# Kernel optimization log

Hardware: AMD Instinct MI355X
Metric: run time of the kernel (lower is better)

## Reference

```python
import jax, jax.numpy as jnp
import numpy as np

B, K, C, G = 8192, 4096, 4096, 32
EPS = 1e-5


def setup_inputs() -> dict:
    key = jax.random.key(0)
    ks = jax.random.split(key, 4)
    x = jax.random.normal(ks[0], (B, K), dtype=jnp.float32)
    weight = jax.random.normal(ks[1], (C, K), dtype=jnp.float32) * (1.0 / np.sqrt(K))
    bias = jax.random.normal(ks[2], (C,), dtype=jnp.float32) * 0.02
    gn_weight = jnp.ones((C,), dtype=jnp.float32)
    gn_bias = jnp.zeros((C,), dtype=jnp.float32)
    multiply_weight = jax.random.normal(ks[3], (C,), dtype=jnp.float32)
    return {"x": x, "weight": weight, "bias": bias, "gn_weight": gn_weight,
            "gn_bias": gn_bias, "multiply_weight": multiply_weight}


def reference(x, weight, bias, gn_weight, gn_bias, multiply_weight):
    # Linear: y = x @ W^T + b   -> [B, C]
    h = jnp.einsum('bk,ck->bc', x, weight) + bias
    # GroupNorm over each group of C//G channels, per sample
    hg = h.reshape(B, G, C // G)
    mean = jnp.mean(hg, axis=-1, keepdims=True)
    var = jnp.mean(jnp.square(hg), axis=-1, keepdims=True) - jnp.square(mean)
    hn = ((hg - mean) * jax.lax.rsqrt(var + EPS)).reshape(B, C)
    hn = hn * gn_weight + gn_bias
    # Swish -> * multiply_weight -> Swish
    x1 = hn * jax.nn.sigmoid(hn)
    x2 = x1 * multiply_weight
    return x2 * jax.nn.sigmoid(x2)
```

## Files before the change

kernel.cpp:

```cpp
#include <hip/hip_runtime.h>


typedef short bf16x8 __attribute__((ext_vector_type(8)));
typedef unsigned short u16x8 __attribute__((ext_vector_type(8)));
typedef unsigned short u16x4 __attribute__((ext_vector_type(4)));
typedef float fx4 __attribute__((ext_vector_type(4)));

__device__ __forceinline__ unsigned short f2bf(float f) {
    union { float f; unsigned u; } v; v.f = f;
    unsigned r = v.u + 0x7FFFu + ((v.u >> 16) & 1u);
    return (unsigned short)(r >> 16);
}

__device__ __forceinline__ void load_lds16(const void* g, void* l) {
    __builtin_amdgcn_global_load_lds(
        (const __attribute__((address_space(1))) void*)g,
        (__attribute__((address_space(3))) void*)l, 16, 0, 0);
}

__global__ void __launch_bounds__(256)
cvt_f32_bf16(const float* __restrict__ src, unsigned short* __restrict__ dst, long long n) {
    long long i = ((long long)blockIdx.x * 256 + threadIdx.x) * 8;
    if (i >= n) return;
    float4 a = *(const float4*)(src + i);
    float4 b = *(const float4*)(src + i + 4);
    u16x8 o;
    o[0] = f2bf(a.x); o[1] = f2bf(a.y); o[2] = f2bf(a.z); o[3] = f2bf(a.w);
    o[4] = f2bf(b.x); o[5] = f2bf(b.y); o[6] = f2bf(b.z); o[7] = f2bf(b.w);
    *(u16x8*)(dst + i) = o;
}

__device__ __forceinline__ void
epilogue(fx4 (&acc)[4][4],
         const float* __restrict__ bias, const float* __restrict__ gnw,
         const float* __restrict__ gnb,  const float* __restrict__ mw,
         float* __restrict__ out, int m0, int n0,
         int wm, int wn, int lrow, int q,
         float (*redS)[128], float (*redQ)[128]) {
    constexpr int C = 4096;
    float bia[4], gw[4], gb[4], mwv[4];
    int cidx[4];
    #pragma unroll
    for (int nt = 0; nt < 4; nt++) {
        int c = n0 + wn * 64 + nt * 16 + lrow;
        cidx[nt] = c;
        bia[nt] = bias[c]; gw[nt] = gnw[c]; gb[nt] = gnb[c]; mwv[nt] = mw[c];
    }
    #pragma unroll
    for (int mt = 0; mt < 4; mt++)
        #pragma unroll
        for (int nt = 0; nt < 4; nt++)
            #pragma unroll
            for (int r = 0; r < 4; r++)
                acc[mt][nt][r] += bia[nt];

    float s[4][4], ss[4][4];
    #pragma unroll
    for (int mt = 0; mt < 4; mt++)
        #pragma unroll
        for (int r = 0; r < 4; r++) {
            float a = 0.f, b = 0.f;
            #pragma unroll
            for (int nt = 0; nt < 4; nt++) {
                float v = acc[mt][nt][r];
                a += v; b += v * v;
            }
            s[mt][r] = a; ss[mt][r] = b;
        }
    #pragma unroll
    for (int off = 1; off < 16; off <<= 1)
        #pragma unroll
        for (int mt = 0; mt < 4; mt++)
            #pragma unroll
            for (int r = 0; r < 4; r++) {
                s[mt][r]  += __shfl_xor(s[mt][r],  off, 64);
                ss[mt][r] += __shfl_xor(ss[mt][r], off, 64);
            }
    if (lrow == 0) {
        #pragma unroll
        for (int mt = 0; mt < 4; mt++)
            #pragma unroll
            for (int r = 0; r < 4; r++) {
                int row = wm * 64 + mt * 16 + q * 4 + r;
                redS[wn][row] = s[mt][r];
                redQ[wn][row] = ss[mt][r];
            }
    }
    __syncthreads();

    #pragma unroll
    for (int mt = 0; mt < 4; mt++)
        #pragma unroll
        for (int r = 0; r < 4; r++) {
            int row = wm * 64 + mt * 16 + q * 4 + r;
            float tot  = redS[0][row] + redS[1][row];
            float tq   = redQ[0][row] + redQ[1][row];
            float mean = tot * (1.0f / 128.0f);
            float var  = tq * (1.0f / 128.0f) - mean * mean;
            s[mt][r]  = mean;
            ss[mt][r] = rsqrtf(var + 1e-5f);
        }

    #pragma unroll
    for (int mt = 0; mt < 4; mt++)
        #pragma unroll
        for (int r = 0; r < 4; r++) {
            size_t row = (size_t)(m0 + wm * 64 + mt * 16 + q * 4 + r);
            #pragma unroll
            for (int nt = 0; nt < 4; nt++) {
                float h  = acc[mt][nt][r];
                float hn = (h - s[mt][r]) * ss[mt][r];
                hn = hn * gw[nt] + gb[nt];
                float x1 = hn / (1.0f + __expf(-hn));
                float x2 = x1 * mwv[nt];
                float y  = x2 / (1.0f + __expf(-x2));
                out[row * (size_t)C + cidx[nt]] = y;
            }
        }
}

__global__ void __launch_bounds__(256)
gemm_bf16(const unsigned short* __restrict__ X,
          const unsigned short* __restrict__ Wt,
          const float* __restrict__ bias, const float* __restrict__ gnw,
          const float* __restrict__ gnb,  const float* __restrict__ mw,
          float* __restrict__ out)
{
    constexpr int K = 4096;
    __shared__ __align__(16) unsigned short As[128 * 32];
    __shared__ __align__(16) unsigned short Bs[128 * 32];
    __shared__ float redS[2][128];
    __shared__ float redQ[2][128];

    const int tid  = threadIdx.x;
    const int wave = tid >> 6;
    const int lane = tid & 63;
    const int wm = wave >> 1, wn = wave & 1;
    const int lrow = lane & 15;
    const int q    = lane >> 4;

    const int m0 = blockIdx.y * 128;
    const int n0 = blockIdx.x * 128;

    const int r0 = tid >> 2;
    const int kk = (tid & 3) * 8;
    const unsigned short* pA0 = X  + (size_t)(m0 + r0) * K + kk;
    const unsigned short* pA1 = X  + (size_t)(m0 + 64 + r0) * K + kk;
    const unsigned short* pB0 = Wt + (size_t)(n0 + r0) * K + kk;
    const unsigned short* pB1 = Wt + (size_t)(n0 + 64 + r0) * K + kk;
    unsigned short* ldsA0 = &As[wave * 512];
    unsigned short* ldsA1 = &As[2048 + wave * 512];
    unsigned short* ldsB0 = &Bs[wave * 512];
    unsigned short* ldsB1 = &Bs[2048 + wave * 512];

    fx4 acc[4][4];
    const fx4 zero = {0.f, 0.f, 0.f, 0.f};
    #pragma unroll
    for (int i = 0; i < 4; i++)
        #pragma unroll
        for (int j = 0; j < 4; j++) acc[i][j] = zero;

    for (int k0 = 0; k0 < K; k0 += 32) {
        load_lds16(pA0 + k0, ldsA0);
        load_lds16(pA1 + k0, ldsA1);
        load_lds16(pB0 + k0, ldsB0);
        load_lds16(pB1 + k0, ldsB1);
        __syncthreads();

        bf16x8 af[4], bfr[4];
        #pragma unroll
        for (int mt = 0; mt < 4; mt++)
            af[mt] = *(const bf16x8*)&As[(wm * 64 + mt * 16 + lrow) * 32 + q * 8];
        #pragma unroll
        for (int nt = 0; nt < 4; nt++)
            bfr[nt] = *(const bf16x8*)&Bs[(wn * 64 + nt * 16 + lrow) * 32 + q * 8];

        #pragma unroll
        for (int mt = 0; mt < 4; mt++)
            #pragma unroll
            for (int nt = 0; nt < 4; nt++)
                acc[mt][nt] = __builtin_amdgcn_mfma_f32_16x16x32_bf16(
                    af[mt], bfr[nt], acc[mt][nt], 0, 0, 0);
        __syncthreads();
    }

    epilogue(acc, bias, gnw, gnb, mw, out, m0, n0, wm, wn, lrow, q, redS, redQ);
}

__global__ void __launch_bounds__(256)
gemm_f32cvt(const float* __restrict__ X, const float* __restrict__ Wt,
            const float* __restrict__ bias, const float* __restrict__ gnw,
            const float* __restrict__ gnb,  const float* __restrict__ mw,
            float* __restrict__ out)
{
    constexpr int K = 4096;
    __shared__ __align__(16) unsigned short As[128 * 32];
    __shared__ __align__(16) unsigned short Bs[128 * 32];
    __shared__ float redS[2][128];
    __shared__ float redQ[2][128];

    const int tid  = threadIdx.x;
    const int wave = tid >> 6;
    const int lane = tid & 63;
    const int wm = wave >> 1, wn = wave & 1;
    const int lrow = lane & 15;
    const int q    = lane >> 4;

    const int m0 = blockIdx.y * 128;
    const int n0 = blockIdx.x * 128;

    const int srow = tid >> 3;
    const int sk   = (tid & 7) * 4;

    fx4 acc[4][4];
    const fx4 zero = {0.f, 0.f, 0.f, 0.f};
    #pragma unroll
    for (int i = 0; i < 4; i++)
        #pragma unroll
        for (int j = 0; j < 4; j++) acc[i][j] = zero;

    for (int k0 = 0; k0 < K; k0 += 32) {
        #pragma unroll
        for (int j = 0; j < 4; j++) {
            int row = j * 32 + srow;
            float4 va = *(const float4*)(X  + (size_t)(m0 + row) * K + k0 + sk);
            float4 vb = *(const float4*)(Wt + (size_t)(n0 + row) * K + k0 + sk);
            u16x4 oa = { f2bf(va.x), f2bf(va.y), f2bf(va.z), f2bf(va.w) };
            u16x4 ob = { f2bf(vb.x), f2bf(vb.y), f2bf(vb.z), f2bf(vb.w) };
            *(u16x4*)&As[row * 32 + sk] = oa;
            *(u16x4*)&Bs[row * 32 + sk] = ob;
        }
        __syncthreads();

        bf16x8 af[4], bfr[4];
        #pragma unroll
        for (int mt = 0; mt < 4; mt++)
            af[mt] = *(const bf16x8*)&As[(wm * 64 + mt * 16 + lrow) * 32 + q * 8];
        #pragma unroll
        for (int nt = 0; nt < 4; nt++)
            bfr[nt] = *(const bf16x8*)&Bs[(wn * 64 + nt * 16 + lrow) * 32 + q * 8];

        #pragma unroll
        for (int mt = 0; mt < 4; mt++)
            #pragma unroll
            for (int nt = 0; nt < 4; nt++)
                acc[mt][nt] = __builtin_amdgcn_mfma_f32_16x16x32_bf16(
                    af[mt], bfr[nt], acc[mt][nt], 0, 0, 0);
        __syncthreads();
    }

    epilogue(acc, bias, gnw, gnb, mw, out, m0, n0, wm, wn, lrow, q, redS, redQ);
}

extern "C" void kernel_launch(void* const* d_in, const int* in_sizes, int n_in,
                              void* d_out, int out_size, void* d_ws, size_t ws_size,
                              hipStream_t stream) {
    (void)in_sizes; (void)n_in; (void)out_size;
    const float* X    = (const float*)d_in[0];
    const float* Wt   = (const float*)d_in[1];
    const float* bias = (const float*)d_in[2];
    const float* gnw  = (const float*)d_in[3];
    const float* gnb  = (const float*)d_in[4];
    const float* mw   = (const float*)d_in[5];
    float* out = (float*)d_out;

    const long long nX = 8192LL * 4096LL;
    const long long nW = 4096LL * 4096LL;
    const size_t need = (size_t)(nX + nW) * 2;

    dim3 grid(4096 / 128, 8192 / 128);

    if (ws_size >= need) {
        unsigned short* Xb = (unsigned short*)d_ws;
        unsigned short* Wb = Xb + nX;
        cvt_f32_bf16<<<(int)(nX / 8 / 256), 256, 0, stream>>>(X,  Xb, nX);
        cvt_f32_bf16<<<(int)(nW / 8 / 256), 256, 0, stream>>>(Wt, Wb, nW);
        gemm_bf16<<<grid, 256, 0, stream>>>(Xb, Wb, bias, gnw, gnb, mw, out);
    } else {
        gemm_f32cvt<<<grid, 256, 0, stream>>>(X, Wt, bias, gnw, gnb, mw, out);
    }
}
```

Before: 648.3 us.

## Replace bf16 GEMM with 256x256-tile pipelined kernel and merged conversion

Replaces the 128x128 single-buffered bf16 GEMM with a 256x256-tile, 512-thread kernel that triple-stages K tiles in LDS through direct global-to-LDS loads. It uses an XOR swizzle against bank conflicts, split barriers with explicit waitcnt, setprio around MFMA bursts, and a block-index swizzle for L2 locality. The two fp32-to-bf16 conversion launches are merged into one. The aim is more data reuse per tile and overlap of loads with MFMA work. In exchange, register and LDS pressure rise (128 KB LDS, 128 accumulator floats per thread), and the hand-written sync is fragile.

```diff
diff --git a/kernel.cpp b/kernel.cpp
--- a/kernel.cpp
+++ b/kernel.cpp
@@ -19,24 +19,223 @@
 }
 
 __global__ void __launch_bounds__(256)
-cvt_f32_bf16(const float* __restrict__ src, unsigned short* __restrict__ dst, long long n) {
+cvt_both(const float* __restrict__ X, const float* __restrict__ W,
+         unsigned short* __restrict__ Xb, unsigned short* __restrict__ Wb,
+         long long nX, long long nW) {
     long long i = ((long long)blockIdx.x * 256 + threadIdx.x) * 8;
-    if (i >= n) return;
-    float4 a = *(const float4*)(src + i);
-    float4 b = *(const float4*)(src + i + 4);
+    const float* src; unsigned short* dst; long long j;
+    if (i < nX) { src = X; dst = Xb; j = i; }
+    else { j = i - nX; if (j >= nW) return; src = W; dst = Wb; }
+    float4 a = *(const float4*)(src + j);
+    float4 b = *(const float4*)(src + j + 4);
     u16x8 o;
     o[0] = f2bf(a.x); o[1] = f2bf(a.y); o[2] = f2bf(a.z); o[3] = f2bf(a.w);
     o[4] = f2bf(b.x); o[5] = f2bf(b.y); o[6] = f2bf(b.z); o[7] = f2bf(b.w);
-    *(u16x8*)(dst + i) = o;
+    *(u16x8*)(dst + j) = o;
+}
+
+#define BAR()    do { __builtin_amdgcn_s_barrier(); asm volatile("" ::: "memory"); } while (0)
+#define LGKM0()  asm volatile("s_waitcnt lgkmcnt(0)" ::: "memory")
+#define VMCNT(n) asm volatile("s_waitcnt vmcnt(" #n ")" ::: "memory")
+
+__global__ void __launch_bounds__(512, 2)
+gemm256(const unsigned short* __restrict__ X,
+        const unsigned short* __restrict__ Wt,
+        const float* __restrict__ bias, const float* __restrict__ gnw,
+        const float* __restrict__ gnb,  const float* __restrict__ mw,
+        float* __restrict__ out)
+{
+    constexpr int Kd = 4096;
+    constexpr int NT = 64;
+    __shared__ __align__(16) unsigned short As[32768];
+    __shared__ __align__(16) unsigned short Bs[32768];
+
+    const int tid  = threadIdx.x;
+    const int w    = tid >> 6;
+    const int lane = tid & 63;
+    const int wm = w >> 2, wn = w & 3;
+    const int lrow = lane & 15, q = lane >> 4;
+
+    const int bid = blockIdx.x;
+    const int swz = (bid & 7) * 64 + (bid >> 3);
+    const int n0 = (swz & 15) * 256;
+    const int m0 = (swz >> 4) * 256;
+
+    const unsigned short* Atile = X  + (size_t)m0 * Kd;
+    const unsigned short* Btile = Wt + (size_t)n0 * Kd;
+
+    const int srow0 = w * 16 + (lane >> 2);
+    const int skc   = (lane & 3) ^ ((srow0 >> 1) & 3);
+    const size_t soff0 = (size_t)srow0 * Kd + skc * 8;
+    const size_t soff1 = soff0 + (size_t)128 * Kd;
+
+    const int fsw  = q ^ ((lrow >> 1) & 3);
+    const int aoff = (wm * 128 + lrow) * 32 + fsw * 8;
+    const int boff = (wn * 64  + lrow) * 32 + fsw * 8;
+
+    fx4 acc[8][4];
+    const fx4 zero = {0.f, 0.f, 0.f, 0.f};
+    #pragma unroll
+    for (int i = 0; i < 8; i++)
+        #pragma unroll
+        for (int j = 0; j < 4; j++) acc[i][j] = zero;
+
+    bf16x8 fa[4], fb[4];
+
+#define STAGE(gt, reg) do { \
+    load_lds16((gt) + soff0, (reg) + w * 512); \
+    load_lds16((gt) + soff1, (reg) + 4096 + w * 512); \
+} while (0)
+
+#define LDA4(regbase, MH) do { \
+    _Pragma("unroll") \
+    for (int _i = 0; _i < 4; _i++) \
+        fa[_i] = *(const bf16x8*)((regbase) + aoff + (MH) * 2048 + _i * 512); \
+} while (0)
+
+#define LDB4(regbase) do { \
+    _Pragma("unroll") \
+    for (int _j = 0; _j < 4; _j++) \
+        fb[_j] = *(const bf16x8*)((regbase) + boff + _j * 512); \
+} while (0)
+
+#define MMA(MH) do { \
+    __builtin_amdgcn_s_setprio(1); \
+    _Pragma("unroll") \
+    for (int _i = 0; _i < 4; _i++) \
+        _Pragma("unroll") \
+        for (int _j = 0; _j < 4; _j++) \
+            acc[(MH)*4+_i][_j] = __builtin_amdgcn_mfma_f32_16x16x32_bf16( \
+                fa[_i], fb[_j], acc[(MH)*4+_i][_j], 0, 0, 0); \
+    __builtin_amdgcn_s_setprio(0); \
+} while (0)
+
+#define KTILE(BUF, ktv) do { \
+    unsigned short* A0  = As + (BUF) * 16384; \
+    unsigned short* A1  = A0 + 8192; \
+    unsigned short* B0  = Bs + (BUF) * 16384; \
+    unsigned short* B1  = B0 + 8192; \
+    unsigned short* nA1 = As + ((BUF) ^ 1) * 16384 + 8192; \
+    unsigned short* nB1 = Bs + ((BUF) ^ 1) * 16384 + 8192; \
+    int _j1 = (ktv) + 1; if (_j1 > NT - 1) _j1 = NT - 1; \
+    int _j2 = (ktv) + 2; if (_j2 > NT - 1) _j2 = NT - 1; \
+     \
+    LDB4(B0); LDA4(A0, 0); \
+    STAGE(Atile + _j1 * 64 + 32, nA1); \
+    BAR(); LGKM0(); MMA(0); BAR(); \
+     \
+    LDA4(A0, 1); \
+    STAGE(Btile + _j1 * 64 + 32, nB1); \
+    BAR(); LGKM0(); MMA(1); BAR(); \
+     \
+    LDB4(B1); LDA4(A1, 0); \
+    STAGE(Atile + _j2 * 64, A0); \
+    BAR(); LGKM0(); MMA(0); BAR(); \
+     \
+    LDA4(A1, 1); \
+    STAGE(Btile + _j2 * 64, B0); \
+    BAR(); LGKM0(); MMA(1); \
+    VMCNT(4); BAR(); \
+} while (0)
+
+    STAGE(Atile + 0,  As + 0);
+    STAGE(Btile + 0,  Bs + 0);
+    STAGE(Atile + 32, As + 8192);
+    STAGE(Btile + 32, Bs + 8192);
+    STAGE(Atile + 64, As + 16384);
+    STAGE(Btile + 64, Bs + 16384);
+    VMCNT(4); BAR();
+
+    #pragma unroll 1
+    for (int kt = 0; kt < NT; kt += 2) {
+        KTILE(0, kt);
+        KTILE(1, kt + 1);
+    }
+
+    VMCNT(0); BAR();
+
+    float* redS = (float*)As;
+    float* redQ = (float*)As + 1024;
+
+    float bia[4], gwv[4], gbv[4], mwv[4]; int cdx[4];
+    #pragma unroll
+    for (int nt = 0; nt < 4; nt++) {
+        int c = n0 + wn * 64 + nt * 16 + lrow;
+        cdx[nt] = c;
+        bia[nt] = bias[c]; gwv[nt] = gnw[c]; gbv[nt] = gnb[c]; mwv[nt] = mw[c];
+    }
+    #pragma unroll
+    for (int mt = 0; mt < 8; mt++)
+        #pragma unroll
+        for (int nt = 0; nt < 4; nt++)
+            #pragma unroll
+            for (int r = 0; r < 4; r++)
+                acc[mt][nt][r] += bia[nt];
+
+    #pragma unroll
+    for (int mt = 0; mt < 8; mt++) {
+        float sv[4], qv[4];
+        #pragma unroll
+        for (int r = 0; r < 4; r++) {
+            float a = 0.f, b = 0.f;
+            #pragma unroll
+            for (int nt = 0; nt < 4; nt++) { float v = acc[mt][nt][r]; a += v; b += v * v; }
+            sv[r] = a; qv[r] = b;
+        }
+        #pragma unroll
+        for (int off = 1; off < 16; off <<= 1)
+            #pragma unroll
+            for (int r = 0; r < 4; r++) {
+                sv[r] += __shfl_xor(sv[r], off, 64);
+                qv[r] += __shfl_xor(qv[r], off, 64);
+            }
+        if (lrow == 0) {
+            #pragma unroll
+            for (int r = 0; r < 4; r++) {
+                redS[w * 128 + mt * 16 + q * 4 + r] = sv[r];
+                redQ[w * 128 + mt * 16 + q * 4 + r] = qv[r];
+            }
+        }
+    }
+    __syncthreads();
+
+    const int pw = w ^ 1;
+    #pragma unroll
+    for (int mt = 0; mt < 8; mt++) {
+        #pragma unroll
+        for (int r = 0; r < 4; r++) {
+            int ri = mt * 16 + q * 4 + r;
+            float tot = redS[w * 128 + ri] + redS[pw * 128 + ri];
+            float tq  = redQ[w * 128 + ri] + redQ[pw * 128 + ri];
+            float mean = tot * (1.0f / 128.0f);
+            float rstd = rsqrtf(tq * (1.0f / 128.0f) - mean * mean + 1e-5f);
+            size_t row = (size_t)(m0 + wm * 128 + mt * 16 + q * 4 + r);
+            float* orow = out + row * 4096;
+            #pragma unroll
+            for (int nt = 0; nt < 4; nt++) {
+                float h  = acc[mt][nt][r];
+                float hn = (h - mean) * rstd;
+                hn = hn * gwv[nt] + gbv[nt];
+                float x1 = hn / (1.0f + __expf(-hn));
+                float x2 = x1 * mwv[nt];
+                orow[cdx[nt]] = x2 / (1.0f + __expf(-x2));
+            }
+        }
+    }
+#undef STAGE
+#undef LDA4
+#undef LDB4
+#undef MMA
+#undef KTILE
 }
 
 __device__ __forceinline__ void
-epilogue(fx4 (&acc)[4][4],
-         const float* __restrict__ bias, const float* __restrict__ gnw,
-         const float* __restrict__ gnb,  const float* __restrict__ mw,
-         float* __restrict__ out, int m0, int n0,
-         int wm, int wn, int lrow, int q,
-         float (*redS)[128], float (*redQ)[128]) {
+epilogue_f(fx4 (&acc)[4][4],
+           const float* __restrict__ bias, const float* __restrict__ gnw,
+           const float* __restrict__ gnb,  const float* __restrict__ mw,
+           float* __restrict__ out, int m0, int n0,
+           int wm, int wn, int lrow, int q,
+           float (*redS)[128], float (*redQ)[128]) {
     constexpr int C = 4096;
     float bia[4], gw[4], gb[4], mwv[4];
     int cidx[4];
@@ -117,74 +316,6 @@
                 out[row * (size_t)C + cidx[nt]] = y;
             }
         }
-}
-
-__global__ void __launch_bounds__(256)
-gemm_bf16(const unsigned short* __restrict__ X,
-          const unsigned short* __restrict__ Wt,
-          const float* __restrict__ bias, const float* __restrict__ gnw,
-          const float* __restrict__ gnb,  const float* __restrict__ mw,
-          float* __restrict__ out)
-{
-    constexpr int K = 4096;
-    __shared__ __align__(16) unsigned short As[128 * 32];
-    __shared__ __align__(16) unsigned short Bs[128 * 32];
-    __shared__ float redS[2][128];
-    __shared__ float redQ[2][128];
-
-    const int tid  = threadIdx.x;
-    const int wave = tid >> 6;
-    const int lane = tid & 63;
-    const int wm = wave >> 1, wn = wave & 1;
-    const int lrow = lane & 15;
-    const int q    = lane >> 4;
-
-    const int m0 = blockIdx.y * 128;
-    const int n0 = blockIdx.x * 128;
-
-    const int r0 = tid >> 2;
-    const int kk = (tid & 3) * 8;
-    const unsigned short* pA0 = X  + (size_t)(m0 + r0) * K + kk;
-    const unsigned short* pA1 = X  + (size_t)(m0 + 64 + r0) * K + kk;
-    const unsigned short* pB0 = Wt + (size_t)(n0 + r0) * K + kk;
-    const unsigned short* pB1 = Wt + (size_t)(n0 + 64 + r0) * K + kk;
-    unsigned short* ldsA0 = &As[wave * 512];
-    unsigned short* ldsA1 = &As[2048 + wave * 512];
-    unsigned short* ldsB0 = &Bs[wave * 512];
-    unsigned short* ldsB1 = &Bs[2048 + wave * 512];
-
-    fx4 acc[4][4];
-    const fx4 zero = {0.f, 0.f, 0.f, 0.f};
-    #pragma unroll
-    for (int i = 0; i < 4; i++)
-        #pragma unroll
-        for (int j = 0; j < 4; j++) acc[i][j] = zero;
-
-    for (int k0 = 0; k0 < K; k0 += 32) {
-        load_lds16(pA0 + k0, ldsA0);
-        load_lds16(pA1 + k0, ldsA1);
-        load_lds16(pB0 + k0, ldsB0);
-        load_lds16(pB1 + k0, ldsB1);
-        __syncthreads();
-
-        bf16x8 af[4], bfr[4];
-        #pragma unroll
-        for (int mt = 0; mt < 4; mt++)
-            af[mt] = *(const bf16x8*)&As[(wm * 64 + mt * 16 + lrow) * 32 + q * 8];
-        #pragma unroll
-        for (int nt = 0; nt < 4; nt++)
-            bfr[nt] = *(const bf16x8*)&Bs[(wn * 64 + nt * 16 + lrow) * 32 + q * 8];
-
-        #pragma unroll
-        for (int mt = 0; mt < 4; mt++)
-            #pragma unroll
-            for (int nt = 0; nt < 4; nt++)
-                acc[mt][nt] = __builtin_amdgcn_mfma_f32_16x16x32_bf16(
-                    af[mt], bfr[nt], acc[mt][nt], 0, 0, 0);
-        __syncthreads();
-    }
-
-    epilogue(acc, bias, gnw, gnb, mw, out, m0, n0, wm, wn, lrow, q, redS, redQ);
 }
 
 __global__ void __launch_bounds__(256)
@@ -249,7 +380,7 @@
         __syncthreads();
     }
 
-    epilogue(acc, bias, gnw, gnb, mw, out, m0, n0, wm, wn, lrow, q, redS, redQ);
+    epilogue_f(acc, bias, gnw, gnb, mw, out, m0, n0, wm, wn, lrow, q, redS, redQ);
 }
 
 extern "C" void kernel_launch(void* const* d_in, const int* in_sizes, int n_in,
@@ -268,15 +399,13 @@
     const long long nW = 4096LL * 4096LL;
     const size_t need = (size_t)(nX + nW) * 2;
 
-    dim3 grid(4096 / 128, 8192 / 128);
-
     if (ws_size >= need) {
         unsigned short* Xb = (unsigned short*)d_ws;
         unsigned short* Wb = Xb + nX;
-        cvt_f32_bf16<<<(int)(nX / 8 / 256), 256, 0, stream>>>(X,  Xb, nX);
-        cvt_f32_bf16<<<(int)(nW / 8 / 256), 256, 0, stream>>>(Wt, Wb, nW);
-        gemm_bf16<<<grid, 256, 0, stream>>>(Xb, Wb, bias, gnw, gnb, mw, out);
+        cvt_both<<<(int)((nX + nW) / 8 / 256), 256, 0, stream>>>(X, Wt, Xb, Wb, nX, nW);
+        gemm256<<<512, 512, 0, stream>>>(Xb, Wb, bias, gnw, gnb, mw, out);
     } else {
+        dim3 grid(4096 / 128, 8192 / 128);
         gemm_f32cvt<<<grid, 256, 0, stream>>>(X, Wt, bias, gnw, gnb, mw, out);
     }
 }
```

After: 540.7 us. 1.2x faster.
